# Kernel tuning notes

Measured on AMD Instinct MI355X. Metric: run time of the kernel, lower is better.

The kernel has to match this reference:

```python
import jax, jax.numpy as jnp
import numpy as np

N_NODES = 50000


def gcn_conv(x, row, col, W, b):
    """PyG GCNConv: add self-loops, symmetric deg^-1/2 normalization,
    linear transform, scatter-add aggregation, bias.
    Self-loop contribution is added analytically (norm = dinv[i]^2)
    instead of appending edges."""
    n = x.shape[0]
    h = x @ W  # [N, out]
    # degree over edges-with-self-loops, counted at target (col)
    deg = jnp.zeros((n,), dtype=x.dtype).at[col].add(1.0) + 1.0
    dinv = jax.lax.rsqrt(deg)  # deg >= 1 thanks to self-loops
    norm = dinv[row] * dinv[col]  # [E]
    # neighbor aggregation: out[col] += norm * h[row]
    agg = jnp.zeros_like(h).at[col].add(norm[:, None] * h[row])
    # self-loop term: dinv[i]^2 * h[i]
    agg = agg + (dinv * dinv)[:, None] * h
    return agg + b


def setup_inputs() -> dict:
    key = jax.random.key(0)
    ks = jax.random.split(key, 8)
    d_in, d_hid, d_out = 128, 128, 128
    n_edges = 625000
    x = jax.random.normal(ks[0], (N_NODES, d_in), dtype=jnp.float32)
    edge_index = jax.random.randint(ks[1], (2, n_edges), 0, N_NODES, dtype=jnp.int64)
    # Glorot-style weights, zero bias (PyG GCNConv defaults)
    def glorot(k, fan_in, fan_out):
        s = jnp.sqrt(6.0 / (fan_in + fan_out)).astype(jnp.float32)
        return jax.random.uniform(k, (fan_in, fan_out), dtype=jnp.float32, minval=-s, maxval=s)
    return {
        "x": x,
        "edge_index": edge_index,
        "W1": glorot(ks[2], d_in, d_hid), "b1": jnp.zeros((d_hid,), jnp.float32),
        "W2": glorot(ks[3], d_hid, d_hid), "b2": jnp.zeros((d_hid,), jnp.float32),
        "W3": glorot(ks[4], d_hid, d_out), "b3": jnp.zeros((d_out,), jnp.float32),
    }


def reference(x, edge_index, W1, b1, W2, b2, W3, b3):
    row, col = edge_index[0], edge_index[1]
    h = jax.nn.relu(gcn_conv(x, row, col, W1, b1))
    h = jax.nn.relu(gcn_conv(h, row, col, W2, b2))
    out = gcn_conv(h, row, col, W3, b3)  # no ReLU on last layer
    return out
```

## Files before the change

kernel.cpp:

```cpp
#include <hip/hip_runtime.h>
#include <hip/hip_fp16.h>

#define NN 50000
#define NE 625000
#define D 128
#define SCAN_BLK 1024
#define NSB ((NN + SCAN_BLK - 1) / SCAN_BLK)


__global__ void zero_kernel(int4* __restrict__ p) {
    int i = blockIdx.x * blockDim.x + threadIdx.x;
    if (i < NN / 4 + 1) p[i] = make_int4(0, 0, 0, 0);
}

__global__ void count_kernel(const int* __restrict__ col, int* __restrict__ counts) {
    int i = blockIdx.x * blockDim.x + threadIdx.x;
    if (i < NE) atomicAdd(&counts[col[i]], 1);
}

__global__ __launch_bounds__(256) void scan1_kernel(const int* __restrict__ counts,
                                                    int* __restrict__ excl,
                                                    int* __restrict__ blocksums) {
    const int b = blockIdx.x, t = threadIdx.x;
    const int base = b * SCAN_BLK + t * 4;
    int v0 = 0, v1 = 0, v2 = 0, v3 = 0;
    if (base + 3 < NN) {
        int4 c = *(const int4*)(counts + base);
        v0 = c.x; v1 = c.y; v2 = c.z; v3 = c.w;
    } else {
        if (base     < NN) v0 = counts[base];
        if (base + 1 < NN) v1 = counts[base + 1];
        if (base + 2 < NN) v2 = counts[base + 2];
        if (base + 3 < NN) v3 = counts[base + 3];
    }
    const int s = v0 + v1 + v2 + v3;
    const int lane = t & 63, wid = t >> 6;
    int inc = s;
    #pragma unroll
    for (int off = 1; off < 64; off <<= 1) {
        int n = __shfl_up(inc, off, 64);
        if (lane >= off) inc += n;
    }
    __shared__ int wsum[4];
    if (lane == 63) wsum[wid] = inc;
    __syncthreads();
    int wbase = 0;
    for (int w = 0; w < wid; w++) wbase += wsum[w];
    const int texcl = wbase + inc - s;
    if (base     < NN) excl[base]     = texcl;
    if (base + 1 < NN) excl[base + 1] = texcl + v0;
    if (base + 2 < NN) excl[base + 2] = texcl + v0 + v1;
    if (base + 3 < NN) excl[base + 3] = texcl + v0 + v1 + v2;
    if (t == 255) blocksums[b] = wbase + inc;
}

__global__ __launch_bounds__(64) void scan2_kernel(const int* __restrict__ blocksums,
                                                   int* __restrict__ blockoff) {
    const int t = threadIdx.x;
    int v = (t < NSB) ? blocksums[t] : 0;
    int inc = v;
    #pragma unroll
    for (int off = 1; off < 64; off <<= 1) {
        int n = __shfl_up(inc, off, 64);
        if (t >= off) inc += n;
    }
    if (t < NSB) blockoff[t] = inc - v;
}

__global__ void scan3_kernel(const int* __restrict__ counts, const int* __restrict__ excl,
                             const int* __restrict__ blockoff, int* __restrict__ offsets,
                             int* __restrict__ cursor, float* __restrict__ dinv) {
    const int i = blockIdx.x * blockDim.x + threadIdx.x;
    if (i < NN) {
        const int o = excl[i] + blockoff[i >> 10];
        offsets[i] = o;
        cursor[i] = o;
        dinv[i] = rsqrtf((float)counts[i] + 1.0f);
    }
    if (i == 0) offsets[NN] = NE;
}

__global__ void fill_kernel(const int* __restrict__ row, const int* __restrict__ col,
                            const float* __restrict__ dinv, int* __restrict__ cursor,
                            uint32_t* __restrict__ csr) {
    int i = blockIdx.x * blockDim.x + threadIdx.x;
    if (i < NE) {
        int r = row[i], c = col[i];
        int p = atomicAdd(&cursor[c], 1);
        __half hw = __float2half_rn(dinv[r] * dinv[c]);
        csr[p] = (uint32_t)r | ((uint32_t)*(const unsigned short*)&hw << 16);
    }
}


__global__ __launch_bounds__(256) void gemm_kernel(const float* __restrict__ A,
                                                   const float* __restrict__ W,
                                                   uint32_t* __restrict__ Hh) {
    __shared__ float Ws[128 * 128];
    const int t = threadIdx.x;
    const int row0 = blockIdx.x * 128;

    const float4* W4 = (const float4*)W;
    float4* Ws4 = (float4*)Ws;
    #pragma unroll 4
    for (int i = t; i < 4096; i += 256) Ws4[i] = W4[i];
    __syncthreads();

    const int rg = t >> 4;
    const int jc = t & 15;
    const float4* A4 = (const float4*)A;
    int aoff[8];
    #pragma unroll
    for (int m = 0; m < 8; m++) {
        int gr = row0 + 8 * rg + m;
        if (gr >= NN) gr = NN - 1;
        aoff[m] = gr * 32;
    }

    float acc[8][8];
    #pragma unroll
    for (int m = 0; m < 8; m++)
        #pragma unroll
        for (int c = 0; c < 8; c++) acc[m][c] = 0.0f;

    for (int k4 = 0; k4 < 32; k4++) {
        float4 a[8];
        #pragma unroll
        for (int m = 0; m < 8; m++) a[m] = A4[aoff[m] + k4];
        #pragma unroll
        for (int kk = 0; kk < 4; kk++) {
            int k = 4 * k4 + kk;
            float4 w0 = Ws4[k * 32 + jc * 2];
            float4 w1 = Ws4[k * 32 + jc * 2 + 1];
            #pragma unroll
            for (int m = 0; m < 8; m++) {
                float av = (kk == 0) ? a[m].x : (kk == 1) ? a[m].y
                         : (kk == 2) ? a[m].z : a[m].w;
                acc[m][0] += av * w0.x;
                acc[m][1] += av * w0.y;
                acc[m][2] += av * w0.z;
                acc[m][3] += av * w0.w;
                acc[m][4] += av * w1.x;
                acc[m][5] += av * w1.y;
                acc[m][6] += av * w1.z;
                acc[m][7] += av * w1.w;
            }
        }
    }

    #pragma unroll
    for (int m = 0; m < 8; m++) {
        int gr = row0 + 8 * rg + m;
        if (gr < NN) {
            __half2 h0 = __float22half2_rn(make_float2(acc[m][0], acc[m][1]));
            __half2 h1 = __float22half2_rn(make_float2(acc[m][2], acc[m][3]));
            __half2 h2 = __float22half2_rn(make_float2(acc[m][4], acc[m][5]));
            __half2 h3 = __float22half2_rn(make_float2(acc[m][6], acc[m][7]));
            uint4 p;
            p.x = *(const uint32_t*)&h0;
            p.y = *(const uint32_t*)&h1;
            p.z = *(const uint32_t*)&h2;
            p.w = *(const uint32_t*)&h3;
            *(uint4*)(Hh + (size_t)gr * 64 + jc * 4) = p;
        }
    }
}


static __device__ __forceinline__ void proc_edge(uint32_t rec, bool valid, int lh,
                                                 const uint2* __restrict__ hh2,
                                                 float4& acc) {
    const int s = (int)(rec & 0xffffu);
    unsigned short wb = (unsigned short)(rec >> 16);
    float w = valid ? __half2float(*(const __half*)&wb) : 0.0f;
    uint2 v = hh2[(size_t)s * 32 + lh];
    float2 lo = __half22float2(*(const __half2*)&v.x);
    float2 hi = __half22float2(*(const __half2*)&v.y);
    acc.x += w * lo.x;
    acc.y += w * lo.y;
    acc.z += w * hi.x;
    acc.w += w * hi.y;
}

__global__ __launch_bounds__(256) void agg_kernel(const uint2* __restrict__ hh2,
                                                  const int* __restrict__ offsets,
                                                  const uint32_t* __restrict__ csr,
                                                  const float* __restrict__ dinv,
                                                  const float* __restrict__ bias,
                                                  float* __restrict__ out,
                                                  const int relu) {
    const int node = blockIdx.x * 4 + (threadIdx.x >> 6);
    if (node >= NN) return;
    const int l = threadIdx.x & 63;
    const int half = l >> 5, lh = l & 31;
    const float di = dinv[node];
    const float sw = di * di;
    const int e0 = offsets[node];
    const int e1 = offsets[node + 1];

    float4 acc0 = make_float4(0.f, 0.f, 0.f, 0.f);
    float4 acc1 = make_float4(0.f, 0.f, 0.f, 0.f);
    float4 acc2 = make_float4(0.f, 0.f, 0.f, 0.f);
    float4 acc3 = make_float4(0.f, 0.f, 0.f, 0.f);

    if (e0 < e1) {
        const int elast = e1 - 1;
        uint32_t r0 = csr[min(e0 + 0 + half, elast)];
        uint32_t r1 = csr[min(e0 + 2 + half, elast)];
        uint32_t r2 = csr[min(e0 + 4 + half, elast)];
        uint32_t r3 = csr[min(e0 + 6 + half, elast)];
        for (int eb = e0; eb < e1; eb += 8) {
            const int nb = eb + 8;
            uint32_t n0 = csr[min(nb + 0 + half, elast)];
            uint32_t n1 = csr[min(nb + 2 + half, elast)];
            uint32_t n2 = csr[min(nb + 4 + half, elast)];
            uint32_t n3 = csr[min(nb + 6 + half, elast)];
            proc_edge(r0, eb + 0 + half < e1, lh, hh2, acc0);
            proc_edge(r1, eb + 2 + half < e1, lh, hh2, acc1);
            proc_edge(r2, eb + 4 + half < e1, lh, hh2, acc2);
            proc_edge(r3, eb + 6 + half < e1, lh, hh2, acc3);
            r0 = n0; r1 = n1; r2 = n2; r3 = n3;
        }
    }

    float4 s;
    s.x = (acc0.x + acc1.x) + (acc2.x + acc3.x);
    s.y = (acc0.y + acc1.y) + (acc2.y + acc3.y);
    s.z = (acc0.z + acc1.z) + (acc2.z + acc3.z);
    s.w = (acc0.w + acc1.w) + (acc2.w + acc3.w);
    s.x += __shfl_xor(s.x, 32, 64);
    s.y += __shfl_xor(s.y, 32, 64);
    s.z += __shfl_xor(s.z, 32, 64);
    s.w += __shfl_xor(s.w, 32, 64);

    uint2 sv = hh2[(size_t)node * 32 + lh];
    float2 slo = __half22float2(*(const __half2*)&sv.x);
    float2 shi = __half22float2(*(const __half2*)&sv.y);
    float4 bv = ((const float4*)bias)[lh];
    s.x += sw * slo.x + bv.x;
    s.y += sw * slo.y + bv.y;
    s.z += sw * shi.x + bv.z;
    s.w += sw * shi.y + bv.w;
    if (relu) {
        s.x = fmaxf(s.x, 0.f);
        s.y = fmaxf(s.y, 0.f);
        s.z = fmaxf(s.z, 0.f);
        s.w = fmaxf(s.w, 0.f);
    }
    if (half == 0) ((float4*)out)[(size_t)node * 32 + lh] = s;
}


extern "C" void kernel_launch(void* const* d_in, const int* in_sizes, int n_in,
                              void* d_out, int out_size, void* d_ws, size_t ws_size,
                              hipStream_t stream) {
    (void)in_sizes; (void)n_in; (void)out_size; (void)ws_size;
    const float* x  = (const float*)d_in[0];
    const int*   ei = (const int*)d_in[1];
    const float* W1 = (const float*)d_in[2];
    const float* b1 = (const float*)d_in[3];
    const float* W2 = (const float*)d_in[4];
    const float* b2 = (const float*)d_in[5];
    const float* W3 = (const float*)d_in[6];
    const float* b3 = (const float*)d_in[7];
    const int* row = ei;
    const int* col = ei + NE;
    float* outp = (float*)d_out;

    char* ws = (char*)d_ws;
    size_t off = 0;
    auto walloc = [&](size_t bytes) -> void* {
        void* p = ws + off;
        off = (off + bytes + 255) & ~(size_t)255;
        return p;
    };
    int*      counts   = (int*)walloc(NN * 4 + 16);
    int*      excl     = (int*)walloc(NN * 4);
    int*      blocksums= (int*)walloc(NSB * 4);
    int*      blockoff = (int*)walloc(NSB * 4);
    int*      offsets  = (int*)walloc((NN + 1) * 4);
    int*      cursor   = (int*)walloc(NN * 4);
    float*    dinv     = (float*)walloc(NN * 4);
    uint32_t* csr      = (uint32_t*)walloc((size_t)NE * 4);
    float*    act      = (float*)walloc((size_t)NN * D * 4);
    uint32_t* hh16     = (uint32_t*)walloc((size_t)NN * D * 2);

    zero_kernel<<<(NN / 4 + 1 + 255) / 256, 256, 0, stream>>>((int4*)counts);
    count_kernel<<<(NE + 255) / 256, 256, 0, stream>>>(col, counts);
    scan1_kernel<<<NSB, 256, 0, stream>>>(counts, excl, blocksums);
    scan2_kernel<<<1, 64, 0, stream>>>(blocksums, blockoff);
    scan3_kernel<<<(NN + 255) / 256, 256, 0, stream>>>(counts, excl, blockoff,
                                                       offsets, cursor, dinv);
    fill_kernel<<<(NE + 255) / 256, 256, 0, stream>>>(row, col, dinv, cursor, csr);

    const int gblocks = (NN + 127) / 128;
    const int ablocks = (NN + 3) / 4;
    const uint2* hh2 = (const uint2*)hh16;
    gemm_kernel<<<gblocks, 256, 0, stream>>>(x, W1, hh16);
    agg_kernel<<<ablocks, 256, 0, stream>>>(hh2, offsets, csr, dinv, b1, act, 1);
    gemm_kernel<<<gblocks, 256, 0, stream>>>(act, W2, hh16);
    agg_kernel<<<ablocks, 256, 0, stream>>>(hh2, offsets, csr, dinv, b2, act, 1);
    gemm_kernel<<<gblocks, 256, 0, stream>>>(act, W3, hh16);
    agg_kernel<<<ablocks, 256, 0, stream>>>(hh2, offsets, csr, dinv, b3, outp, 0);
}
```

Measured before the change: 245.9 us.

## Use fp16 MFMA GEMM with prepacked weights and fp16 intermediate activations

Replaces the FP32 FMA-based dense transform with a matrix-core kernel using 16x16x32 fp16 MFMA, with weights pre-packed into the fragment layout by a small packing kernel. Output tiles are staged through shared memory for coalesced fp16 stores. The aggregation kernel now writes fp16 activations for hidden layers, halving the activation traffic read by the next GEMM. Inputs and weights are rounded to fp16 before multiplication, which lowers precision.

```diff
diff --git a/kernel.cpp b/kernel.cpp
--- a/kernel.cpp
+++ b/kernel.cpp
@@ -6,6 +6,11 @@
 #define D 128
 #define SCAN_BLK 1024
 #define NSB ((NN + SCAN_BLK - 1) / SCAN_BLK)
+
+typedef _Float16 half8 __attribute__((ext_vector_type(8)));
+typedef float f32x4 __attribute__((ext_vector_type(4)));
+
+union H8U4 { _Float16 h[8]; uint4 u; };
 
 
 __global__ void zero_kernel(int4* __restrict__ p) {
@@ -93,75 +98,104 @@
 }
 
 
-__global__ __launch_bounds__(256) void gemm_kernel(const float* __restrict__ A,
-                                                   const float* __restrict__ W,
-                                                   uint32_t* __restrict__ Hh) {
-    __shared__ float Ws[128 * 128];
+__global__ __launch_bounds__(256) void wpack_kernel(const float* __restrict__ W,
+                                                    uint4* __restrict__ wp) {
+    int t = blockIdx.x * blockDim.x + threadIdx.x;
+    if (t >= 2048) return;
+    int lane = t & 63, entry = t >> 6;
+    int ks = entry >> 3, ctg = entry & 7;
+    int j = ctg * 16 + (lane & 15);
+    int kb = ks * 32 + (lane >> 4) * 8;
+    H8U4 u;
+    #pragma unroll
+    for (int e = 0; e < 8; e++) u.h[e] = (_Float16)W[(kb + e) * 128 + j];
+    wp[t] = u.u;
+}
+
+
+template <bool IN_F16>
+__global__ __launch_bounds__(256) void gemm_mfma(const void* __restrict__ Ain,
+                                                 const uint4* __restrict__ wpack,
+                                                 uint32_t* __restrict__ Hh) {
+    __shared__ alignas(16) _Float16 Cs[64][152];
     const int t = threadIdx.x;
-    const int row0 = blockIdx.x * 128;
-
-    const float4* W4 = (const float4*)W;
-    float4* Ws4 = (float4*)Ws;
-    #pragma unroll 4
-    for (int i = t; i < 4096; i += 256) Ws4[i] = W4[i];
+    const int w = t >> 6, l = t & 63;
+    const int row0 = blockIdx.x * 64;
+    const int lr = l & 15;
+    const int lg = l >> 4;
+
+    int arow[4];
+    #pragma unroll
+    for (int rt = 0; rt < 4; rt++) {
+        int gr = row0 + rt * 16 + lr;
+        arow[rt] = (gr < NN) ? gr : NN - 1;
+    }
+
+    f32x4 acc[4][2];
+    #pragma unroll
+    for (int rt = 0; rt < 4; rt++)
+        #pragma unroll
+        for (int ct = 0; ct < 2; ct++)
+            acc[rt][ct] = (f32x4){0.f, 0.f, 0.f, 0.f};
+
+    #pragma unroll
+    for (int ks = 0; ks < 4; ks++) {
+        const int kbase = ks * 32 + lg * 8;
+        half8 af[4];
+        if (IN_F16) {
+            const uint4* A = (const uint4*)Ain;
+            #pragma unroll
+            for (int rt = 0; rt < 4; rt++) {
+                H8U4 u;
+                u.u = A[arow[rt] * 16 + (kbase >> 3)];
+                af[rt] = *(half8*)u.h;
+            }
+        } else {
+            const float4* A = (const float4*)Ain;
+            #pragma unroll
+            for (int rt = 0; rt < 4; rt++) {
+                float4 p0 = A[arow[rt] * 32 + (kbase >> 2)];
+                float4 p1 = A[arow[rt] * 32 + (kbase >> 2) + 1];
+                half8 h;
+                h[0] = (_Float16)p0.x; h[1] = (_Float16)p0.y;
+                h[2] = (_Float16)p0.z; h[3] = (_Float16)p0.w;
+                h[4] = (_Float16)p1.x; h[5] = (_Float16)p1.y;
+                h[6] = (_Float16)p1.z; h[7] = (_Float16)p1.w;
+                af[rt] = h;
+            }
+        }
+        half8 bf[2];
+        #pragma unroll
+        for (int ct = 0; ct < 2; ct++) {
+            H8U4 u;
+            u.u = wpack[(ks * 8 + (w * 2 + ct)) * 64 + l];
+            bf[ct] = *(half8*)u.h;
+        }
+        #pragma unroll
+        for (int rt = 0; rt < 4; rt++)
+            #pragma unroll
+            for (int ct = 0; ct < 2; ct++)
+                acc[rt][ct] = __builtin_amdgcn_mfma_f32_16x16x32_f16(
+                    af[rt], bf[ct], acc[rt][ct], 0, 0, 0);
+    }
+
+    #pragma unroll
+    for (int rt = 0; rt < 4; rt++)
+        #pragma unroll
+        for (int ct = 0; ct < 2; ct++) {
+            const int col = w * 32 + ct * 16 + lr;
+            #pragma unroll
+            for (int r = 0; r < 4; r++)
+                Cs[rt * 16 + lg * 4 + r][col] = (_Float16)acc[rt][ct][r];
+        }
     __syncthreads();
 
-    const int rg = t >> 4;
-    const int jc = t & 15;
-    const float4* A4 = (const float4*)A;
-    int aoff[8];
-    #pragma unroll
-    for (int m = 0; m < 8; m++) {
-        int gr = row0 + 8 * rg + m;
-        if (gr >= NN) gr = NN - 1;
-        aoff[m] = gr * 32;
-    }
-
-    float acc[8][8];
-    #pragma unroll
-    for (int m = 0; m < 8; m++)
-        #pragma unroll
-        for (int c = 0; c < 8; c++) acc[m][c] = 0.0f;
-
-    for (int k4 = 0; k4 < 32; k4++) {
-        float4 a[8];
-        #pragma unroll
-        for (int m = 0; m < 8; m++) a[m] = A4[aoff[m] + k4];
-        #pragma unroll
-        for (int kk = 0; kk < 4; kk++) {
-            int k = 4 * k4 + kk;
-            float4 w0 = Ws4[k * 32 + jc * 2];
-            float4 w1 = Ws4[k * 32 + jc * 2 + 1];
-            #pragma unroll
-            for (int m = 0; m < 8; m++) {
-                float av = (kk == 0) ? a[m].x : (kk == 1) ? a[m].y
-                         : (kk == 2) ? a[m].z : a[m].w;
-                acc[m][0] += av * w0.x;
-                acc[m][1] += av * w0.y;
-                acc[m][2] += av * w0.z;
-                acc[m][3] += av * w0.w;
-                acc[m][4] += av * w1.x;
-                acc[m][5] += av * w1.y;
-                acc[m][6] += av * w1.z;
-                acc[m][7] += av * w1.w;
-            }
-        }
-    }
-
-    #pragma unroll
-    for (int m = 0; m < 8; m++) {
-        int gr = row0 + 8 * rg + m;
-        if (gr < NN) {
-            __half2 h0 = __float22half2_rn(make_float2(acc[m][0], acc[m][1]));
-            __half2 h1 = __float22half2_rn(make_float2(acc[m][2], acc[m][3]));
-            __half2 h2 = __float22half2_rn(make_float2(acc[m][4], acc[m][5]));
-            __half2 h3 = __float22half2_rn(make_float2(acc[m][6], acc[m][7]));
-            uint4 p;
-            p.x = *(const uint32_t*)&h0;
-            p.y = *(const uint32_t*)&h1;
-            p.z = *(const uint32_t*)&h2;
-            p.w = *(const uint32_t*)&h3;
-            *(uint4*)(Hh + (size_t)gr * 64 + jc * 4) = p;
+    #pragma unroll
+    for (int i = t; i < 1024; i += 256) {
+        const int row = i >> 4, c16 = i & 15;
+        if (row0 + row < NN) {
+            uint4 u = *(const uint4*)&Cs[row][c16 * 8];
+            *(uint4*)(Hh + (size_t)(row0 + row) * 64 + c16 * 4) = u;
         }
     }
 }
@@ -182,12 +216,13 @@
     acc.w += w * hi.y;
 }
 
+template <bool OUT_F16>
 __global__ __launch_bounds__(256) void agg_kernel(const uint2* __restrict__ hh2,
                                                   const int* __restrict__ offsets,
                                                   const uint32_t* __restrict__ csr,
                                                   const float* __restrict__ dinv,
                                                   const float* __restrict__ bias,
-                                                  float* __restrict__ out,
+                                                  void* __restrict__ out,
                                                   const int relu) {
     const int node = blockIdx.x * 4 + (threadIdx.x >> 6);
     if (node >= NN) return;
@@ -247,7 +282,16 @@
         s.z = fmaxf(s.z, 0.f);
         s.w = fmaxf(s.w, 0.f);
     }
-    if (half == 0) ((float4*)out)[(size_t)node * 32 + lh] = s;
+    if (half == 0) {
+        if (OUT_F16) {
+            __half2 p0 = __float22half2_rn(make_float2(s.x, s.y));
+            __half2 p1 = __float22half2_rn(make_float2(s.z, s.w));
+            uint2 u = make_uint2(*(const uint32_t*)&p0, *(const uint32_t*)&p1);
+            *(uint2*)((uint32_t*)out + (size_t)node * 64 + lh * 2) = u;
+        } else {
+            ((float4*)out)[(size_t)node * 32 + lh] = s;
+        }
+    }
 }
 
 
@@ -282,8 +326,11 @@
     int*      cursor   = (int*)walloc(NN * 4);
     float*    dinv     = (float*)walloc(NN * 4);
     uint32_t* csr      = (uint32_t*)walloc((size_t)NE * 4);
-    float*    act      = (float*)walloc((size_t)NN * D * 4);
+    uint32_t* act16    = (uint32_t*)walloc((size_t)NN * D * 2);
     uint32_t* hh16     = (uint32_t*)walloc((size_t)NN * D * 2);
+    uint4*    wp1      = (uint4*)walloc(2048 * 16);
+    uint4*    wp2      = (uint4*)walloc(2048 * 16);
+    uint4*    wp3      = (uint4*)walloc(2048 * 16);
 
     zero_kernel<<<(NN / 4 + 1 + 255) / 256, 256, 0, stream>>>((int4*)counts);
     count_kernel<<<(NE + 255) / 256, 256, 0, stream>>>(col, counts);
@@ -292,14 +339,17 @@
     scan3_kernel<<<(NN + 255) / 256, 256, 0, stream>>>(counts, excl, blockoff,
                                                        offsets, cursor, dinv);
     fill_kernel<<<(NE + 255) / 256, 256, 0, stream>>>(row, col, dinv, cursor, csr);
-
-    const int gblocks = (NN + 127) / 128;
+    wpack_kernel<<<8, 256, 0, stream>>>(W1, wp1);
+    wpack_kernel<<<8, 256, 0, stream>>>(W2, wp2);
+    wpack_kernel<<<8, 256, 0, stream>>>(W3, wp3);
+
+    const int gblocks = (NN + 63) / 64;
     const int ablocks = (NN + 3) / 4;
     const uint2* hh2 = (const uint2*)hh16;
-    gemm_kernel<<<gblocks, 256, 0, stream>>>(x, W1, hh16);
-    agg_kernel<<<ablocks, 256, 0, stream>>>(hh2, offsets, csr, dinv, b1, act, 1);
-    gemm_kernel<<<gblocks, 256, 0, stream>>>(act, W2, hh16);
-    agg_kernel<<<ablocks, 256, 0, stream>>>(hh2, offsets, csr, dinv, b2, act, 1);
-    gemm_kernel<<<gblocks, 256, 0, stream>>>(act, W3, hh16);
-    agg_kernel<<<ablocks, 256, 0, stream>>>(hh2, offsets, csr, dinv, b3, outp, 0);
-}
+    gemm_mfma<false><<<gblocks, 256, 0, stream>>>(x, wp1, hh16);
+    agg_kernel<true><<<ablocks, 256, 0, stream>>>(hh2, offsets, csr, dinv, b1, act16, 1);
+    gemm_mfma<true><<<gblocks, 256, 0, stream>>>(act16, wp2, hh16);
+    agg_kernel<true><<<ablocks, 256, 0, stream>>>(hh2, offsets, csr, dinv, b2, act16, 1);
+    gemm_mfma<true><<<gblocks, 256, 0, stream>>>(act16, wp3, hh16);
+    agg_kernel<false><<<ablocks, 256, 0, stream>>>(hh2, offsets, csr, dinv, b3, outp, 0);
+}
```

Result: faster. 215.8 us (-12.2%).
